# Kernel tuning notes

Hardware: AMD Instinct MI355X
Metric: run time of the kernel (lower is better)

Reference implementation:

```python
import jax, jax.numpy as jnp
import numpy as np

ODE_STEPS = 4
LN_EPS = 1e-5


def setup_inputs() -> dict:
    key = jax.random.key(0)
    ks = jax.random.split(key, 18)
    B, L, F, E, H, OH = 256, 1024, 64, 128, 128, 128
    s = lambda n: 1.0 / np.sqrt(n)
    u = lambda k, shp, n: jax.random.uniform(k, shp, jnp.float32, -s(n), s(n))
    return {
        "x": jax.random.normal(ks[0], (B, L, F), jnp.float32),
        "dt": jax.random.uniform(ks[1], (B, L), jnp.float32),
        "mask": jax.random.randint(ks[2], (B, L), 0, 2).astype(jnp.int32),
        # x_proj
        "Wx": u(ks[3], (E, F), F), "bx": u(ks[4], (E,), F),
        # ODEFunc: Linear(H,OH) -> tanh -> Linear(OH,H)
        "W1": u(ks[5], (OH, H), H), "b1": u(ks[6], (OH,), H),
        "W2": u(ks[7], (H, OH), OH), "b2": u(ks[8], (H,), OH),
        # GRUCell
        "W_ih": u(ks[9], (3 * H, E), H), "b_ih": u(ks[10], (3 * H,), H),
        "W_hh": u(ks[11], (3 * H, H), H), "b_hh": u(ks[12], (3 * H,), H),
        # head: LayerNorm + Linear(H,1)
        "ln_g": jnp.ones((H,), jnp.float32), "ln_b": jnp.zeros((H,), jnp.float32),
        "Wh": u(ks[13], (1, H), H), "bh": u(ks[14], (1,), H),
    }


def reference(x, dt, Wx, bx, W1, b1, W2, b2, W_ih, b_ih, W_hh, b_hh,
              ln_g, ln_b, Wh, bh, mask):
    B, L, F = x.shape
    H = W_hh.shape[1]

    def odefunc(h):
        return jnp.tanh(h @ W1.T + b1) @ W2.T + b2

    def ode_euler(h, dte):  # dte: [B]
        step = dte / float(ODE_STEPS)
        for _ in range(ODE_STEPS):
            h = h + step[:, None] * odefunc(h)
        return h

    def gru_cell(xe, h):
        gi = xe @ W_ih.T + b_ih
        gh = h @ W_hh.T + b_hh
        i_r, i_z, i_n = jnp.split(gi, 3, axis=-1)
        h_r, h_z, h_n = jnp.split(gh, 3, axis=-1)
        r = jax.nn.sigmoid(i_r + h_r)
        z = jax.nn.sigmoid(i_z + h_z)
        n = jnp.tanh(i_n + r * h_n)
        return (1.0 - z) * n + z * h

    def step(h, inp):
        xi, dti, mi = inp  # [B,F], [B], [B] int
        mi_f = mi.astype(x.dtype)
        active = jnp.sum(mi_f) > 0  # torch skips step only if ALL masked
        hi = ode_euler(h, dti * mi_f)
        xe = jax.nn.relu(xi @ Wx.T + bx)
        hg = gru_cell(xe, hi)
        h_new = jnp.where(active, hg, h)
        return h_new, h_new

    h0 = jnp.zeros((B, H), x.dtype)
    xs = (jnp.swapaxes(x, 0, 1), dt.T, mask.T)
    _, Hs = jax.lax.scan(step, h0, xs)       # [L,B,H]
    Hs = jnp.swapaxes(Hs, 0, 1)              # [B,L,H]

    mu = jnp.mean(Hs, axis=-1, keepdims=True)
    var = jnp.var(Hs, axis=-1, keepdims=True)
    hn = (Hs - mu) / jnp.sqrt(var + LN_EPS) * ln_g + ln_b
    logits_t = (hn @ Wh.T + bh)[..., 0]      # [B,L]

    mask_f = mask.astype(x.dtype)
    logits_t = logits_t * mask_f
    len_valid = jnp.maximum(jnp.sum(mask_f, axis=1), 1.0)
    return jnp.sum(logits_t, axis=1) / len_valid
```

## Files before the change

### kernel.cpp

```cpp
#include <hip/hip_runtime.h>

#define Bb 256
#define Ll 1024
#define Ff 64
#define Ee 128
#define Hh 128
#define CH 32

typedef _Float16 h2v __attribute__((ext_vector_type(2)));

__device__ __forceinline__ unsigned pack_h2(float a, float b) {
  h2v v; v[0] = (_Float16)a; v[1] = (_Float16)b;
  return __builtin_bit_cast(unsigned, v);
}
__device__ __forceinline__ float dot2(unsigned w, unsigned x, float acc) {
#if defined(__has_builtin) && __has_builtin(__builtin_amdgcn_fdot2)
  return __builtin_amdgcn_fdot2(__builtin_bit_cast(h2v, w),
                                __builtin_bit_cast(h2v, x), acc, false);
#else
  h2v wv = __builtin_bit_cast(h2v, w), xv = __builtin_bit_cast(h2v, x);
  acc = fmaf((float)wv[0], (float)xv[0], acc);
  return fmaf((float)wv[1], (float)xv[1], acc);
#endif
}
__device__ __forceinline__ float dppadd1(float v) {
  int s = __builtin_amdgcn_mov_dpp(__builtin_bit_cast(int, v), 0xB1, 0xF, 0xF, true);
  return v + __builtin_bit_cast(float, s);
}
__device__ __forceinline__ float dppadd2(float v) {
  int s = __builtin_amdgcn_mov_dpp(__builtin_bit_cast(int, v), 0x4E, 0xF, 0xF, true);
  return v + __builtin_bit_cast(float, s);
}
__device__ __forceinline__ float qsum(float a0, float a1) {
  return dppadd2(dppadd1(a0 + a1));
}
__device__ __forceinline__ float fast_tanh(float x) {
  float e = __expf(2.0f * x);
  return 1.0f - 2.0f / (e + 1.0f);
}
__device__ __forceinline__ float fast_sigmoid(float x) {
  return 1.0f / (1.0f + __expf(-x));
}

__device__ __forceinline__ float mv16(const unsigned* __restrict__ w,
                                      const unsigned* __restrict__ v, int q0) {
  float a0 = 0.0f, a1 = 0.0f;
#pragma unroll
  for (int c = 0; c < 4; ++c) {
    const uint4 hv = *(const uint4*)&v[q0 + 4 * c];
    a0 = dot2(w[4*c+0], hv.x, a0); a1 = dot2(w[4*c+1], hv.y, a1);
    a0 = dot2(w[4*c+2], hv.z, a0); a1 = dot2(w[4*c+3], hv.w, a1);
  }
  return qsum(a0, a1);
}
__device__ __forceinline__ float gi_gate(const unsigned* __restrict__ wrow,
                                         const unsigned* __restrict__ xe,
                                         int q0, int swi) {
  float g0 = 0.0f, g1 = 0.0f;
#pragma unroll
  for (int c = 0; c < 4; ++c) {
    const uint4 xv = *(const uint4*)&xe[q0 + 4 * c];
    const uint4 w4 = *(const uint4*)&wrow[(q0 + 4 * c) ^ swi];
    g0 = dot2(w4.x, xv.x, g0); g1 = dot2(w4.y, xv.y, g1);
    g0 = dot2(w4.z, xv.z, g0); g1 = dot2(w4.w, xv.w, g1);
  }
  return qsum(g0, g1);
}

__global__ __launch_bounds__(512, 1) void k_fused(
    const float* __restrict__ x, const float* __restrict__ dtp,
    const int* __restrict__ mask,
    const float* __restrict__ Wx, const float* __restrict__ bx,
    const float* __restrict__ W1, const float* __restrict__ b1,
    const float* __restrict__ W2, const float* __restrict__ b2,
    const float* __restrict__ Wih, const float* __restrict__ bih,
    const float* __restrict__ Whh, const float* __restrict__ bhh,
    const float* __restrict__ lng, const float* __restrict__ lnb,
    const float* __restrict__ Whd, const float* __restrict__ bhp,
    float* __restrict__ out)
{
  const int b = blockIdx.x;
  const int tid = threadIdx.x;
  const int lane = tid & 63;
  const int wv = tid >> 6;
  const int jl = lane >> 2;
  const int ks = lane & 3;
  const int j = (wv << 4) + jl;
  const int q0 = ks << 4;
  const int q0x = ks << 3;
  const int swi = (j & 15) << 2;
  const int swx = (j & 7) << 2;

  __shared__ int act_lds[Ll];
  __shared__ __align__(16) unsigned wih_lds[3 * Hh * 64];
  __shared__ __align__(16) unsigned wx_lds[Hh * 32];
  __shared__ __align__(16) unsigned x16[CH * 32];
  __shared__ __align__(16) unsigned xe16[Ee / 2];
  __shared__ __align__(16) unsigned u16[Hh / 2];
  __shared__ __align__(16) unsigned h16[2][Hh / 2];
  __shared__ float bias_lds[6 * Hh];
  __shared__ float dt_ch[CH];
  __shared__ int   m_ch[CH];
  __shared__ float red_lds[48];
  __shared__ float cc_lds[2];

  for (int t0 = tid; t0 < Ll; t0 += 512) {
    int a = 0;
#pragma unroll 8
    for (int bb = 0; bb < Bb; ++bb) a |= mask[(size_t)bb * Ll + t0];
    act_lds[t0] = a;
  }
  for (int idx = tid; idx < 3 * Hh * 64; idx += 512) {
    const int r = idx >> 6, w = idx & 63;
    wih_lds[(r << 6) | (w ^ ((r & 15) << 2))] =
        pack_h2(Wih[(size_t)r * Ee + 2 * w], Wih[(size_t)r * Ee + 2 * w + 1]);
  }
  for (int idx = tid; idx < Hh * 32; idx += 512) {
    const int r = idx >> 5, w = idx & 31;
    wx_lds[(r << 5) | (w ^ ((r & 7) << 2))] =
        pack_h2(Wx[(size_t)r * Ff + 2 * w], Wx[(size_t)r * Ff + 2 * w + 1]);
  }
  for (int i = tid; i < 3 * Hh; i += 512) {
    bias_lds[i] = bih[i];
    bias_lds[3 * Hh + i] = bhh[i];
  }
  if (tid == 0) {
    float s1 = 0.0f, s0 = 0.0f;
    for (int i = 0; i < Hh; ++i) { s1 += lng[i] * Whd[i]; s0 += lnb[i] * Whd[i]; }
    cc_lds[0] = s1; cc_lds[1] = s0 + bhp[0];
  }
  unsigned w1h[16], w2h[16], whr[16], whz[16], whn[16];
#pragma unroll
  for (int ii = 0; ii < 8; ++ii) {
    float4 a4;
    a4 = *(const float4*)&W1[(size_t)j * Hh + (ks << 5) + 4 * ii];
    w1h[2*ii] = pack_h2(a4.x, a4.y); w1h[2*ii+1] = pack_h2(a4.z, a4.w);
    a4 = *(const float4*)&W2[(size_t)j * Hh + (ks << 5) + 4 * ii];
    w2h[2*ii] = pack_h2(a4.x, a4.y); w2h[2*ii+1] = pack_h2(a4.z, a4.w);
    a4 = *(const float4*)&Whh[(size_t)j * Hh + (ks << 5) + 4 * ii];
    whr[2*ii] = pack_h2(a4.x, a4.y); whr[2*ii+1] = pack_h2(a4.z, a4.w);
    a4 = *(const float4*)&Whh[(size_t)(Hh + j) * Hh + (ks << 5) + 4 * ii];
    whz[2*ii] = pack_h2(a4.x, a4.y); whz[2*ii+1] = pack_h2(a4.z, a4.w);
    a4 = *(const float4*)&Whh[(size_t)(2 * Hh + j) * Hh + (ks << 5) + 4 * ii];
    whn[2*ii] = pack_h2(a4.x, a4.y); whn[2*ii+1] = pack_h2(a4.z, a4.w);
  }
  const float bxj = bx[j];
  const float b1j = b1[j], b2j = b2[j];
  const float gw = lng[j] * Whd[j];

  if (tid < Hh / 2) { h16[0][tid] = 0u; h16[1][tid] = 0u; }
  float hreg = 0.0f, gir = 0.0f, giz = 0.0f, gin = 0.0f;
  float acc = 0.0f, cnt = 0.0f;
  int pp = 0;
  __syncthreads();

#pragma unroll 1
  for (int t = 0; t < Ll; ++t) {
    const int tc = t & (CH - 1);
    if (tc == 0) {
      const int st = tid >> 4, g = tid & 15;
      const float4 a = *(const float4*)(x + ((size_t)b * Ll + t + st) * Ff + g * 4);
      uint2 pk; pk.x = pack_h2(a.x, a.y); pk.y = pack_h2(a.z, a.w);
      *(uint2*)&x16[st * 32 + g * 2] = pk;
      if (tid < CH) dt_ch[tid] = dtp[(size_t)b * Ll + t + tid];
      else if (tid < 2 * CH) m_ch[tid - CH] = mask[(size_t)b * Ll + t + (tid - CH)];
      __syncthreads();
    }
    const float dtv = dt_ch[tc];
    const int m = m_ch[tc];
    const int act = act_lds[t];
    const float stepv = dtv * (float)m * 0.25f;
    unsigned* hcur = h16[pp];

    {
      float p0 = 0.0f, p1 = 0.0f;
      const unsigned* xr = &x16[tc * 32];
      const unsigned* wxr = &wx_lds[j << 5];
#pragma unroll
      for (int c = 0; c < 2; ++c) {
        const uint4 xv = *(const uint4*)&xr[q0x + 4 * c];
        const uint4 w4 = *(const uint4*)&wxr[(q0x + 4 * c) ^ swx];
        p0 = dot2(w4.x, xv.x, p0); p1 = dot2(w4.y, xv.y, p1);
        p0 = dot2(w4.z, xv.z, p0); p1 = dot2(w4.w, xv.w, p1);
      }
      const float xev = fmaxf(qsum(p0, p1) + bxj, 0.0f);
      if (ks == 0) ((_Float16*)xe16)[j] = (_Float16)xev;

      const float uu = fast_tanh(mv16(w1h, hcur, q0) + b1j);
      if (ks == 0) ((_Float16*)u16)[j] = (_Float16)uu;
    }
    __syncthreads();

    {
      hreg = fmaf(stepv, mv16(w2h, u16, q0) + b2j, hreg);
      if (ks == 0) ((_Float16*)hcur)[j] = (_Float16)hreg;
      gir = gi_gate(&wih_lds[j << 6], xe16, q0, swi) + bias_lds[j];
    }
    __syncthreads();

    {
      const float uu = fast_tanh(mv16(w1h, hcur, q0) + b1j);
      if (ks == 0) ((_Float16*)u16)[j] = (_Float16)uu;
      giz = gi_gate(&wih_lds[(Hh + j) << 6], xe16, q0, swi) + bias_lds[Hh + j];
    }
    __syncthreads();
    {
      hreg = fmaf(stepv, mv16(w2h, u16, q0) + b2j, hreg);
      if (ks == 0) ((_Float16*)hcur)[j] = (_Float16)hreg;
      gin = gi_gate(&wih_lds[(2 * Hh + j) << 6], xe16, q0, swi) + bias_lds[2 * Hh + j];
    }
    __syncthreads();

#pragma unroll
    for (int s = 2; s < 4; ++s) {
      {
        const float uu = fast_tanh(mv16(w1h, hcur, q0) + b1j);
        if (ks == 0) ((_Float16*)u16)[j] = (_Float16)uu;
      }
      __syncthreads();
      {
        hreg = fmaf(stepv, mv16(w2h, u16, q0) + b2j, hreg);
        if (ks == 0) ((_Float16*)hcur)[j] = (_Float16)hreg;
      }
      __syncthreads();
    }

    {
      float pr = 0.0f, pz = 0.0f, pn = 0.0f;
#pragma unroll
      for (int c = 0; c < 4; ++c) {
        const uint4 hv = *(const uint4*)&hcur[q0 + 4 * c];
        pr = dot2(whr[4*c+0], hv.x, pr); pr = dot2(whr[4*c+1], hv.y, pr);
        pr = dot2(whr[4*c+2], hv.z, pr); pr = dot2(whr[4*c+3], hv.w, pr);
        pz = dot2(whz[4*c+0], hv.x, pz); pz = dot2(whz[4*c+1], hv.y, pz);
        pz = dot2(whz[4*c+2], hv.z, pz); pz = dot2(whz[4*c+3], hv.w, pz);
        pn = dot2(whn[4*c+0], hv.x, pn); pn = dot2(whn[4*c+1], hv.y, pn);
        pn = dot2(whn[4*c+2], hv.z, pn); pn = dot2(whn[4*c+3], hv.w, pn);
      }
      pr = qsum(pr, 0.0f) + bias_lds[3 * Hh + j];
      pz = qsum(pz, 0.0f) + bias_lds[4 * Hh + j];
      pn = qsum(pn, 0.0f) + bias_lds[5 * Hh + j];
      const float r = fast_sigmoid(gir + pr);
      const float z = fast_sigmoid(giz + pz);
      const float n = fast_tanh(gin + r * pn);
      const float hg = (1.0f - z) * n + z * hreg;
      if (act) hreg = hg;
      if (ks == 0) ((_Float16*)h16[pp ^ 1])[j] = (_Float16)hreg;

      float s1 = hreg, s2 = hreg * hreg, sd = hreg * gw;
#pragma unroll
      for (int o = 4; o <= 16; o <<= 1) {
        s1 += __shfl_xor(s1, o); s2 += __shfl_xor(s2, o); sd += __shfl_xor(sd, o);
      }
      if ((lane & 31) == 0) {
        const int slot = (wv << 1) | (lane >> 5);
        red_lds[slot * 3 + 0] = s1; red_lds[slot * 3 + 1] = s2; red_lds[slot * 3 + 2] = sd;
      }
    }
    __syncthreads();

    if (tid == 0 && m) {
      float S1 = 0.0f, S2 = 0.0f, SD = 0.0f;
#pragma unroll
      for (int q = 0; q < 16; ++q) {
        S1 += red_lds[q * 3 + 0]; S2 += red_lds[q * 3 + 1]; SD += red_lds[q * 3 + 2];
      }
      const float mu = S1 * (1.0f / 128.0f);
      const float var = S2 * (1.0f / 128.0f) - mu * mu;
      const float rstd = rsqrtf(var + 1e-5f);
      acc += rstd * (SD - mu * cc_lds[0]) + cc_lds[1];
      cnt += 1.0f;
    }
    pp ^= 1;
  }

  if (tid == 0) out[b] = acc / fmaxf(cnt, 1.0f);
}

extern "C" void kernel_launch(void* const* d_in, const int* in_sizes, int n_in,
                              void* d_out, int out_size, void* d_ws, size_t ws_size,
                              hipStream_t stream) {
  const float* x    = (const float*)d_in[0];
  const float* dt   = (const float*)d_in[1];
  const int*   mask = (const int*)d_in[2];
  const float* Wx   = (const float*)d_in[3];
  const float* bx   = (const float*)d_in[4];
  const float* W1   = (const float*)d_in[5];
  const float* b1   = (const float*)d_in[6];
  const float* W2   = (const float*)d_in[7];
  const float* b2   = (const float*)d_in[8];
  const float* Wih  = (const float*)d_in[9];
  const float* bih  = (const float*)d_in[10];
  const float* Whh  = (const float*)d_in[11];
  const float* bhh  = (const float*)d_in[12];
  const float* lng  = (const float*)d_in[13];
  const float* lnb  = (const float*)d_in[14];
  const float* Wh   = (const float*)d_in[15];
  const float* bh   = (const float*)d_in[16];
  float* out = (float*)d_out;

  k_fused<<<dim3(Bb), dim3(512), 0, stream>>>(
      x, dt, mask, Wx, bx, W1, b1, W2, b2, Wih, bih, Whh, bhh,
      lng, lnb, Wh, bh, out);
}
```

Before: 3.312 ms.

## Reformulate Euler ODE in pre-activation space with fused W1·W2 and pipeline x/GRU input

A prep kernel precomputes M=W1·W2 and c=W1·b2, so each Euler substep updates the pre-tanh vector v directly (v += step*(M u + c)). Each substep then needs one matvec and one barrier instead of two. h is reconstructed once per timestep from the sum of the u vectors via W2 kept in LDS. The input projection and the GRU input gates for the next timestep are computed ahead, x/dt/mask chunks are double-buffered with prefetch into registers, and the LayerNorm reduction is deferred to the next iteration, which removes further barriers. The change adds fp16 rounding of the fused M and cross-step reordering that may change numerics slightly.

```diff
diff --git a/kernel.cpp b/kernel.cpp
--- a/kernel.cpp
+++ b/kernel.cpp
@@ -2,9 +2,6 @@
 
 #define Bb 256
 #define Ll 1024
-#define Ff 64
-#define Ee 128
-#define Hh 128
 #define CH 32
 
 typedef _Float16 h2v __attribute__((ext_vector_type(2)));
@@ -53,9 +50,9 @@
   }
   return qsum(a0, a1);
 }
-__device__ __forceinline__ float gi_gate(const unsigned* __restrict__ wrow,
-                                         const unsigned* __restrict__ xe,
-                                         int q0, int swi) {
+__device__ __forceinline__ float giq(const unsigned* __restrict__ wrow,
+                                     const unsigned* __restrict__ xe,
+                                     int q0, int swi) {
   float g0 = 0.0f, g1 = 0.0f;
 #pragma unroll
   for (int c = 0; c < 4; ++c) {
@@ -65,6 +62,24 @@
     g0 = dot2(w4.z, xv.z, g0); g1 = dot2(w4.w, xv.w, g1);
   }
   return qsum(g0, g1);
+}
+
+__global__ __launch_bounds__(256) void k_prep(
+    const float* __restrict__ W1, const float* __restrict__ W2,
+    const float* __restrict__ b2, float* __restrict__ ws)
+{
+  const int idx = blockIdx.x * 256 + threadIdx.x;
+  if (idx < 16384) {
+    const int i = idx >> 7, j = idx & 127;
+    float s = 0.f;
+    for (int k = 0; k < 128; ++k) s = fmaf(W1[i * 128 + k], W2[k * 128 + j], s);
+    ws[idx] = s;
+  } else if (idx < 16512) {
+    const int i = idx - 16384;
+    float s = 0.f;
+    for (int k = 0; k < 128; ++k) s = fmaf(W1[i * 128 + k], b2[k], s);
+    ws[idx] = s;
+  }
 }
 
 __global__ __launch_bounds__(512, 1) void k_fused(
@@ -77,8 +92,12 @@
     const float* __restrict__ Whh, const float* __restrict__ bhh,
     const float* __restrict__ lng, const float* __restrict__ lnb,
     const float* __restrict__ Whd, const float* __restrict__ bhp,
+    const float* __restrict__ ws,
     float* __restrict__ out)
 {
+  const float* Mf = ws;
+  const float* cf = ws + 16384;
+
   const int b = blockIdx.x;
   const int tid = threadIdx.x;
   const int lane = tid & 63;
@@ -89,18 +108,18 @@
   const int q0 = ks << 4;
   const int q0x = ks << 3;
   const int swi = (j & 15) << 2;
-  const int swx = (j & 7) << 2;
 
   __shared__ int act_lds[Ll];
-  __shared__ __align__(16) unsigned wih_lds[3 * Hh * 64];
-  __shared__ __align__(16) unsigned wx_lds[Hh * 32];
-  __shared__ __align__(16) unsigned x16[CH * 32];
-  __shared__ __align__(16) unsigned xe16[Ee / 2];
-  __shared__ __align__(16) unsigned u16[Hh / 2];
-  __shared__ __align__(16) unsigned h16[2][Hh / 2];
-  __shared__ float bias_lds[6 * Hh];
-  __shared__ float dt_ch[CH];
-  __shared__ int   m_ch[CH];
+  __shared__ __align__(16) unsigned wih_lds[3 * 128 * 64];
+  __shared__ __align__(16) unsigned w2_lds[128 * 64];
+  __shared__ __align__(16) unsigned x16[2][CH * 32];
+  __shared__ __align__(16) unsigned xe16[64];
+  __shared__ __align__(16) unsigned ubuf[2][64];
+  __shared__ __align__(16) unsigned usumb[64];
+  __shared__ __align__(16) unsigned fb16[64];
+  __shared__ __align__(16) unsigned h16[2][64];
+  __shared__ float dt_ch[2][CH];
+  __shared__ int   m_ch[2][CH];
   __shared__ float red_lds[48];
   __shared__ float cc_lds[2];
 
@@ -110,143 +129,185 @@
     for (int bb = 0; bb < Bb; ++bb) a |= mask[(size_t)bb * Ll + t0];
     act_lds[t0] = a;
   }
-  for (int idx = tid; idx < 3 * Hh * 64; idx += 512) {
+  for (int idx = tid; idx < 3 * 128 * 64; idx += 512) {
     const int r = idx >> 6, w = idx & 63;
     wih_lds[(r << 6) | (w ^ ((r & 15) << 2))] =
-        pack_h2(Wih[(size_t)r * Ee + 2 * w], Wih[(size_t)r * Ee + 2 * w + 1]);
-  }
-  for (int idx = tid; idx < Hh * 32; idx += 512) {
-    const int r = idx >> 5, w = idx & 31;
-    wx_lds[(r << 5) | (w ^ ((r & 7) << 2))] =
-        pack_h2(Wx[(size_t)r * Ff + 2 * w], Wx[(size_t)r * Ff + 2 * w + 1]);
-  }
-  for (int i = tid; i < 3 * Hh; i += 512) {
-    bias_lds[i] = bih[i];
-    bias_lds[3 * Hh + i] = bhh[i];
+        pack_h2(Wih[(size_t)r * 128 + 2 * w], Wih[(size_t)r * 128 + 2 * w + 1]);
+  }
+  for (int idx = tid; idx < 128 * 64; idx += 512) {
+    const int r = idx >> 6, w = idx & 63;
+    w2_lds[(r << 6) | (w ^ ((r & 15) << 2))] =
+        pack_h2(W2[(size_t)r * 128 + 2 * w], W2[(size_t)r * 128 + 2 * w + 1]);
   }
   if (tid == 0) {
-    float s1 = 0.0f, s0 = 0.0f;
-    for (int i = 0; i < Hh; ++i) { s1 += lng[i] * Whd[i]; s0 += lnb[i] * Whd[i]; }
+    float s1 = 0.f, s0 = 0.f;
+    for (int i = 0; i < 128; ++i) { s1 += lng[i] * Whd[i]; s0 += lnb[i] * Whd[i]; }
     cc_lds[0] = s1; cc_lds[1] = s0 + bhp[0];
   }
-  unsigned w1h[16], w2h[16], whr[16], whz[16], whn[16];
+  {
+    const int sl = tid >> 4, part = tid & 15;
+    const float4 a = *(const float4*)(x + ((size_t)b * Ll + sl) * 64 + part * 4);
+    x16[0][sl * 32 + part * 2 + 0] = pack_h2(a.x, a.y);
+    x16[0][sl * 32 + part * 2 + 1] = pack_h2(a.z, a.w);
+    if (tid < CH) dt_ch[0][tid] = dtp[(size_t)b * Ll + tid];
+    else if (tid < 2 * CH) m_ch[0][tid - CH] = mask[(size_t)b * Ll + (tid - CH)];
+  }
+  unsigned w1h[16], mh[16], whr[16], whz[16], whn[16], wxh[8];
 #pragma unroll
   for (int ii = 0; ii < 8; ++ii) {
     float4 a4;
-    a4 = *(const float4*)&W1[(size_t)j * Hh + (ks << 5) + 4 * ii];
+    a4 = *(const float4*)&W1[(size_t)j * 128 + (ks << 5) + 4 * ii];
     w1h[2*ii] = pack_h2(a4.x, a4.y); w1h[2*ii+1] = pack_h2(a4.z, a4.w);
-    a4 = *(const float4*)&W2[(size_t)j * Hh + (ks << 5) + 4 * ii];
-    w2h[2*ii] = pack_h2(a4.x, a4.y); w2h[2*ii+1] = pack_h2(a4.z, a4.w);
-    a4 = *(const float4*)&Whh[(size_t)j * Hh + (ks << 5) + 4 * ii];
+    a4 = *(const float4*)&Mf[(size_t)j * 128 + (ks << 5) + 4 * ii];
+    mh[2*ii] = pack_h2(a4.x, a4.y); mh[2*ii+1] = pack_h2(a4.z, a4.w);
+    a4 = *(const float4*)&Whh[(size_t)j * 128 + (ks << 5) + 4 * ii];
     whr[2*ii] = pack_h2(a4.x, a4.y); whr[2*ii+1] = pack_h2(a4.z, a4.w);
-    a4 = *(const float4*)&Whh[(size_t)(Hh + j) * Hh + (ks << 5) + 4 * ii];
+    a4 = *(const float4*)&Whh[(size_t)(128 + j) * 128 + (ks << 5) + 4 * ii];
     whz[2*ii] = pack_h2(a4.x, a4.y); whz[2*ii+1] = pack_h2(a4.z, a4.w);
-    a4 = *(const float4*)&Whh[(size_t)(2 * Hh + j) * Hh + (ks << 5) + 4 * ii];
+    a4 = *(const float4*)&Whh[(size_t)(256 + j) * 128 + (ks << 5) + 4 * ii];
     whn[2*ii] = pack_h2(a4.x, a4.y); whn[2*ii+1] = pack_h2(a4.z, a4.w);
   }
-  const float bxj = bx[j];
-  const float b1j = b1[j], b2j = b2[j];
+#pragma unroll
+  for (int ii = 0; ii < 4; ++ii) {
+    const float4 a4 = *(const float4*)&Wx[(size_t)j * 64 + (ks << 4) + 4 * ii];
+    wxh[2*ii] = pack_h2(a4.x, a4.y); wxh[2*ii+1] = pack_h2(a4.z, a4.w);
+  }
+  const float bxj = bx[j], b1j = b1[j], b2j = b2[j], cj = cf[j];
+  const float bir = bih[j], biz = bih[128 + j], bin_ = bih[256 + j];
+  const float bhr = bhh[j], bhz = bhh[128 + j], bhn = bhh[256 + j];
   const float gw = lng[j] * Whd[j];
 
-  if (tid < Hh / 2) { h16[0][tid] = 0u; h16[1][tid] = 0u; }
-  float hreg = 0.0f, gir = 0.0f, giz = 0.0f, gin = 0.0f;
-  float acc = 0.0f, cnt = 0.0f;
-  int pp = 0;
+  if (tid < 64) { h16[0][tid] = 0u; h16[1][tid] = 0u; }
+  float hreg = 0.f;
+  float gicr = 0.f, gicz = 0.f, gicn = 0.f;
+  float gnr = 0.f, gnz = 0.f, gnn = 0.f;
+  float accb = 0.f, cntb = 0.f;
+  int mreg = 0;
+  float4 rx0 = {0,0,0,0}; float rdt = 0.f; int rmk = 0;
+  __syncthreads();
+
+  {
+    float p0 = 0.f, p1 = 0.f;
+#pragma unroll
+    for (int c = 0; c < 2; ++c) {
+      const uint4 xv = *(const uint4*)&x16[0][q0x + 4 * c];
+      p0 = dot2(wxh[4*c+0], xv.x, p0); p1 = dot2(wxh[4*c+1], xv.y, p1);
+      p0 = dot2(wxh[4*c+2], xv.z, p0); p1 = dot2(wxh[4*c+3], xv.w, p1);
+    }
+    const float xev = fmaxf(qsum(p0, p1) + bxj, 0.f);
+    if (ks == 0) ((_Float16*)xe16)[j] = (_Float16)xev;
+  }
+  __syncthreads();
+  gicr = giq(&wih_lds[j << 6], xe16, q0, swi) + bir;
+  gicz = giq(&wih_lds[(128 + j) << 6], xe16, q0, swi) + biz;
+  gicn = giq(&wih_lds[(256 + j) << 6], xe16, q0, swi) + bin_;
   __syncthreads();
 
 #pragma unroll 1
   for (int t = 0; t < Ll; ++t) {
-    const int tc = t & (CH - 1);
-    if (tc == 0) {
-      const int st = tid >> 4, g = tid & 15;
-      const float4 a = *(const float4*)(x + ((size_t)b * Ll + t + st) * Ff + g * 4);
-      uint2 pk; pk.x = pack_h2(a.x, a.y); pk.y = pack_h2(a.z, a.w);
-      *(uint2*)&x16[st * 32 + g * 2] = pk;
-      if (tid < CH) dt_ch[tid] = dtp[(size_t)b * Ll + t + tid];
-      else if (tid < 2 * CH) m_ch[tid - CH] = mask[(size_t)b * Ll + t + (tid - CH)];
-      __syncthreads();
-    }
-    const float dtv = dt_ch[tc];
-    const int m = m_ch[tc];
-    const int act = act_lds[t];
-    const float stepv = dtv * (float)m * 0.25f;
-    unsigned* hcur = h16[pp];
-
-    {
-      float p0 = 0.0f, p1 = 0.0f;
-      const unsigned* xr = &x16[tc * 32];
-      const unsigned* wxr = &wx_lds[j << 5];
-#pragma unroll
-      for (int c = 0; c < 2; ++c) {
-        const uint4 xv = *(const uint4*)&xr[q0x + 4 * c];
-        const uint4 w4 = *(const uint4*)&wxr[(q0x + 4 * c) ^ swx];
-        p0 = dot2(w4.x, xv.x, p0); p1 = dot2(w4.y, xv.y, p1);
-        p0 = dot2(w4.z, xv.z, p0); p1 = dot2(w4.w, xv.w, p1);
-      }
-      const float xev = fmaxf(qsum(p0, p1) + bxj, 0.0f);
-      if (ks == 0) ((_Float16*)xe16)[j] = (_Float16)xev;
-
-      const float uu = fast_tanh(mv16(w1h, hcur, q0) + b1j);
-      if (ks == 0) ((_Float16*)u16)[j] = (_Float16)uu;
-    }
-    __syncthreads();
-
-    {
-      hreg = fmaf(stepv, mv16(w2h, u16, q0) + b2j, hreg);
-      if (ks == 0) ((_Float16*)hcur)[j] = (_Float16)hreg;
-      gir = gi_gate(&wih_lds[j << 6], xe16, q0, swi) + bias_lds[j];
-    }
-    __syncthreads();
-
-    {
-      const float uu = fast_tanh(mv16(w1h, hcur, q0) + b1j);
-      if (ks == 0) ((_Float16*)u16)[j] = (_Float16)uu;
-      giz = gi_gate(&wih_lds[(Hh + j) << 6], xe16, q0, swi) + bias_lds[Hh + j];
-    }
-    __syncthreads();
-    {
-      hreg = fmaf(stepv, mv16(w2h, u16, q0) + b2j, hreg);
-      if (ks == 0) ((_Float16*)hcur)[j] = (_Float16)hreg;
-      gin = gi_gate(&wih_lds[(2 * Hh + j) << 6], xe16, q0, swi) + bias_lds[2 * Hh + j];
-    }
-    __syncthreads();
-
-#pragma unroll
-    for (int s = 2; s < 4; ++s) {
-      {
-        const float uu = fast_tanh(mv16(w1h, hcur, q0) + b1j);
-        if (ks == 0) ((_Float16*)u16)[j] = (_Float16)uu;
-      }
-      __syncthreads();
-      {
-        hreg = fmaf(stepv, mv16(w2h, u16, q0) + b2j, hreg);
-        if (ks == 0) ((_Float16*)hcur)[j] = (_Float16)hreg;
-      }
-      __syncthreads();
-    }
-
-    {
-      float pr = 0.0f, pz = 0.0f, pn = 0.0f;
-#pragma unroll
-      for (int c = 0; c < 4; ++c) {
-        const uint4 hv = *(const uint4*)&hcur[q0 + 4 * c];
-        pr = dot2(whr[4*c+0], hv.x, pr); pr = dot2(whr[4*c+1], hv.y, pr);
-        pr = dot2(whr[4*c+2], hv.z, pr); pr = dot2(whr[4*c+3], hv.w, pr);
-        pz = dot2(whz[4*c+0], hv.x, pz); pz = dot2(whz[4*c+1], hv.y, pz);
-        pz = dot2(whz[4*c+2], hv.z, pz); pz = dot2(whz[4*c+3], hv.w, pz);
-        pn = dot2(whn[4*c+0], hv.x, pn); pn = dot2(whn[4*c+1], hv.y, pn);
-        pn = dot2(whn[4*c+2], hv.z, pn); pn = dot2(whn[4*c+3], hv.w, pn);
-      }
-      pr = qsum(pr, 0.0f) + bias_lds[3 * Hh + j];
-      pz = qsum(pz, 0.0f) + bias_lds[4 * Hh + j];
-      pn = qsum(pn, 0.0f) + bias_lds[5 * Hh + j];
-      const float r = fast_sigmoid(gir + pr);
-      const float z = fast_sigmoid(giz + pz);
-      const float n = fast_tanh(gin + r * pn);
-      const float hg = (1.0f - z) * n + z * hreg;
-      if (act) hreg = hg;
-      if (ks == 0) ((_Float16*)h16[pp ^ 1])[j] = (_Float16)hreg;
-
+    const int cb = (t >> 5) & 1, tc = t & 31;
+    const float sv = dt_ch[cb][tc] * (float)m_ch[cb][tc] * 0.25f;
+    const unsigned* hb = h16[t & 1];
+    const int refill = (tc == 16) && ((t >> 5) < 31);
+
+    float v, usum;
+
+    {
+      if (refill) {
+        const int sl = tid >> 4, part = tid & 15;
+        rx0 = *(const float4*)(x + ((size_t)b * Ll + ((t >> 5) + 1) * 32 + sl) * 64 + part * 4);
+        if (tid < CH) rdt = dtp[(size_t)b * Ll + ((t >> 5) + 1) * 32 + tid];
+        else if (tid < 2 * CH) rmk = mask[(size_t)b * Ll + ((t >> 5) + 1) * 32 + (tid - CH)];
+      }
+      v = mv16(w1h, hb, q0);
+      const float u0 = fast_tanh(v + b1j);
+      usum = u0;
+      if (ks == 0) ((_Float16*)ubuf[0])[j] = (_Float16)u0;
+      if (t + 1 < Ll) {
+        const int nb2 = ((t + 1) >> 5) & 1, ns = (t + 1) & 31;
+        float p0 = 0.f, p1 = 0.f;
+#pragma unroll
+        for (int c = 0; c < 2; ++c) {
+          const uint4 xv = *(const uint4*)&x16[nb2][ns * 32 + q0x + 4 * c];
+          p0 = dot2(wxh[4*c+0], xv.x, p0); p1 = dot2(wxh[4*c+1], xv.y, p1);
+          p0 = dot2(wxh[4*c+2], xv.z, p0); p1 = dot2(wxh[4*c+3], xv.w, p1);
+        }
+        const float xev = fmaxf(qsum(p0, p1) + bxj, 0.f);
+        if (ks == 0) ((_Float16*)xe16)[j] = (_Float16)xev;
+      }
+      if (tid == 0 && t > 0) {
+        float S1 = 0.f, S2 = 0.f, SD = 0.f;
+#pragma unroll
+        for (int q = 0; q < 16; ++q) {
+          S1 += red_lds[q * 3 + 0]; S2 += red_lds[q * 3 + 1]; SD += red_lds[q * 3 + 2];
+        }
+        if (mreg) {
+          const float mu = S1 * (1.0f / 128.0f);
+          const float var = S2 * (1.0f / 128.0f) - mu * mu;
+          const float rstd = rsqrtf(var + 1e-5f);
+          accb += rstd * (SD - mu * cc_lds[0]) + cc_lds[1];
+          cntb += 1.f;
+        }
+      }
+    }
+    __syncthreads();
+
+    {
+      const float t2 = mv16(mh, ubuf[0], q0);
+      v = fmaf(sv, t2 + cj, v);
+      const float u1 = fast_tanh(v + b1j);
+      usum += u1;
+      if (ks == 0) ((_Float16*)ubuf[1])[j] = (_Float16)u1;
+      gnr = giq(&wih_lds[j << 6], xe16, q0, swi) + bir;
+    }
+    __syncthreads();
+
+    {
+      const float t2 = mv16(mh, ubuf[1], q0);
+      v = fmaf(sv, t2 + cj, v);
+      const float u2 = fast_tanh(v + b1j);
+      usum += u2;
+      if (ks == 0) ((_Float16*)ubuf[0])[j] = (_Float16)u2;
+      gnz = giq(&wih_lds[(128 + j) << 6], xe16, q0, swi) + biz;
+    }
+    __syncthreads();
+
+    {
+      const float t2 = mv16(mh, ubuf[0], q0);
+      v = fmaf(sv, t2 + cj, v);
+      const float u3 = fast_tanh(v + b1j);
+      usum += u3;
+      if (ks == 0) ((_Float16*)usumb)[j] = (_Float16)usum;
+      gnn = giq(&wih_lds[(256 + j) << 6], xe16, q0, swi) + bin_;
+    }
+    __syncthreads();
+
+    float hf;
+    {
+      const float k2 = giq(&w2_lds[j << 6], usumb, q0, swi);
+      hf = hreg + sv * k2 + 4.f * sv * b2j;
+      if (ks == 0) ((_Float16*)fb16)[j] = (_Float16)hf;
+      if (refill) {
+        const int nb = ((t >> 5) + 1) & 1;
+        const int sl = tid >> 4, part = tid & 15;
+        x16[nb][sl * 32 + part * 2 + 0] = pack_h2(rx0.x, rx0.y);
+        x16[nb][sl * 32 + part * 2 + 1] = pack_h2(rx0.z, rx0.w);
+        if (tid < CH) dt_ch[nb][tid] = rdt;
+        else if (tid < 2 * CH) m_ch[nb][tid - CH] = rmk;
+      }
+    }
+    __syncthreads();
+
+    {
+      const float pr = mv16(whr, fb16, q0) + bhr;
+      const float pz = mv16(whz, fb16, q0) + bhz;
+      const float pn = mv16(whn, fb16, q0) + bhn;
+      const float rr = fast_sigmoid(gicr + pr);
+      const float zz = fast_sigmoid(gicz + pz);
+      const float nn = fast_tanh(gicn + rr * pn);
+      const float hg = (1.f - zz) * nn + zz * hf;
+      hreg = act_lds[t] ? hg : hf;
+      if (ks == 0) ((_Float16*)h16[(t + 1) & 1])[j] = (_Float16)hreg;
       float s1 = hreg, s2 = hreg * hreg, sd = hreg * gw;
 #pragma unroll
       for (int o = 4; o <= 16; o <<= 1) {
@@ -256,25 +317,27 @@
         const int slot = (wv << 1) | (lane >> 5);
         red_lds[slot * 3 + 0] = s1; red_lds[slot * 3 + 1] = s2; red_lds[slot * 3 + 2] = sd;
       }
-    }
-    __syncthreads();
-
-    if (tid == 0 && m) {
-      float S1 = 0.0f, S2 = 0.0f, SD = 0.0f;
-#pragma unroll
-      for (int q = 0; q < 16; ++q) {
-        S1 += red_lds[q * 3 + 0]; S2 += red_lds[q * 3 + 1]; SD += red_lds[q * 3 + 2];
-      }
+      if (tid == 0) mreg = m_ch[cb][tc];
+      gicr = gnr; gicz = gnz; gicn = gnn;
+    }
+    __syncthreads();
+  }
+
+  if (tid == 0) {
+    float S1 = 0.f, S2 = 0.f, SD = 0.f;
+#pragma unroll
+    for (int q = 0; q < 16; ++q) {
+      S1 += red_lds[q * 3 + 0]; S2 += red_lds[q * 3 + 1]; SD += red_lds[q * 3 + 2];
+    }
+    if (mreg) {
       const float mu = S1 * (1.0f / 128.0f);
       const float var = S2 * (1.0f / 128.0f) - mu * mu;
       const float rstd = rsqrtf(var + 1e-5f);
-      acc += rstd * (SD - mu * cc_lds[0]) + cc_lds[1];
-      cnt += 1.0f;
-    }
-    pp ^= 1;
-  }
-
-  if (tid == 0) out[b] = acc / fmaxf(cnt, 1.0f);
+      accb += rstd * (SD - mu * cc_lds[0]) + cc_lds[1];
+      cntb += 1.f;
+    }
+    out[b] = accb / fmaxf(cntb, 1.f);
+  }
 }
 
 extern "C" void kernel_launch(void* const* d_in, const int* in_sizes, int n_in,
@@ -297,9 +360,11 @@
   const float* lnb  = (const float*)d_in[14];
   const float* Wh   = (const float*)d_in[15];
   const float* bh   = (const float*)d_in[16];
+  float* ws = (float*)d_ws;
   float* out = (float*)d_out;
 
+  k_prep<<<dim3(65), dim3(256), 0, stream>>>(W1, W2, b2, ws);
   k_fused<<<dim3(Bb), dim3(512), 0, stream>>>(
       x, dt, mask, Wx, bx, W1, b1, W2, b2, Wih, bih, Whh, bhh,
-      lng, lnb, Wh, bh, out);
-}
+      lng, lnb, Wh, bh, ws, out);
+}
```

Measured after the change: 2.772 ms, median of 2. 1.19x faster.
